# Kernel optimization log

Hardware: AMD Instinct MI355X
Metric: run time of the kernel (lower is better)

Reference implementation:

```python
import jax, jax.numpy as jnp
import numpy as np

N = 32768      # nodes
E = 524288     # edges (avg degree 16)
G = 512        # graphs in batch
F_IN = 64      # one-hot node-label dim
H = 128        # hidden_dim
C = 2          # num_classes (NCI1)
BN_EPS = 1e-3  # keras BatchNormalization default epsilon


def setup_inputs() -> dict:
    key = jax.random.key(0)
    ks = jax.random.split(key, 32)
    d = {}
    d["x"] = jax.random.normal(ks[0], (N, F_IN), jnp.float32)
    d["edge_weight"] = jax.random.uniform(ks[1], (E,), jnp.float32)
    i = 2
    din = F_IN
    for l in range(5):
        d[f"W1_{l}"] = jax.random.normal(ks[i], (din, H), jnp.float32) / np.float32(np.sqrt(din)); i += 1
        d[f"b1_{l}"] = jnp.zeros((H,), jnp.float32)
        d[f"W2_{l}"] = jax.random.normal(ks[i], (H, H), jnp.float32) / np.float32(np.sqrt(H)); i += 1
        d[f"b2_{l}"] = jnp.zeros((H,), jnp.float32)
        din = H
    for j in (1, 2, 3):  # bn1, bn2, bn3 (bn0/bn4 unused in original call())
        d[f"g{j}"] = jnp.ones((H,), jnp.float32)
        d[f"be{j}"] = jnp.zeros((H,), jnp.float32)
        d[f"m{j}"] = jnp.zeros((H,), jnp.float32)
        d[f"v{j}"] = jnp.ones((H,), jnp.float32)
    d["Wm1"] = jax.random.normal(ks[i], (5 * H, 128), jnp.float32) / np.float32(np.sqrt(5 * H)); i += 1
    d["bm1"] = jnp.zeros((128,), jnp.float32)
    d["Wm2"] = jax.random.normal(ks[i], (128, C), jnp.float32) / np.float32(np.sqrt(128.0)); i += 1
    d["bm2"] = jnp.zeros((C,), jnp.float32)
    d["edge_index"] = jax.random.randint(ks[i], (2, E), 0, N, dtype=jnp.int32); i += 1
    d["node_graph_index"] = jnp.sort(jax.random.randint(ks[i], (N,), 0, G, dtype=jnp.int32))
    return d


def reference(x, edge_weight,
              W1_0, b1_0, W2_0, b2_0,
              W1_1, b1_1, W2_1, b2_1,
              W1_2, b1_2, W2_2, b2_2,
              W1_3, b1_3, W2_3, b2_3,
              W1_4, b1_4, W2_4, b2_4,
              g1, be1, m1, v1,
              g2, be2, m2, v2,
              g3, be3, m3, v3,
              Wm1, bm1, Wm2, bm2,
              edge_index, node_graph_index):
    src, dst = edge_index[0], edge_index[1]

    def gin(h, W1, b1, W2, b2):
        # GIN with eps=0: h' = MLP(h + sum_{j in N(i)} w_ij * h_j)
        msg = h[dst] * edge_weight[:, None]              # [E, d]
        agg = jax.ops.segment_sum(msg, src, num_segments=N)
        h2 = h + agg
        return jax.nn.relu(h2 @ W1 + b1) @ W2 + b2

    def bn(h, g, be, m, v):  # inference-mode batchnorm
        return (h - m) * jax.lax.rsqrt(v + BN_EPS) * g + be

    h1 = gin(x, W1_0, b1_0, W2_0, b2_0)
    h2 = gin(bn(h1, g1, be1, m1, v1), W1_1, b1_1, W2_1, b2_1)
    h3 = gin(bn(h2, g1, be1, m1, v1), W1_2, b1_2, W2_2, b2_2)  # bn1 reused, as in source
    h4 = gin(bn(h3, g2, be2, m2, v2), W1_3, b1_3, W2_3, b2_3)
    h5 = gin(bn(h4, g3, be3, m3, v3), W1_4, b1_4, W2_4, b2_4)
    h5 = bn(h5, g3, be3, m3, v3)                                # bn3 reused, as in source

    pool = lambda h: jax.ops.segment_sum(h, node_graph_index, num_segments=G)
    hg = jnp.concatenate([pool(h1), pool(h2), pool(h3), pool(h4), pool(h5)], axis=-1)  # [G, 5H]
    # readout MLP (dropout inactive at inference)
    return jax.nn.relu(hg @ Wm1 + bm1) @ Wm2 + bm2  # [G, C]
```

## Files before the change

kernel.cpp:

```cpp
#include <hip/hip_runtime.h>
#include <hip/hip_bf16.h>

#define NN 32768
#define EE 524288
#define GG 512
#define CAP 48

typedef __bf16 bf16x8 __attribute__((ext_vector_type(8)));
typedef float  f32x4  __attribute__((ext_vector_type(4)));

static __device__ __forceinline__ float bf2f(unsigned short u) {
    union { unsigned int i; float f; } v; v.i = ((unsigned int)u) << 16; return v.f;
}
static __device__ __forceinline__ unsigned short f2bf(float f) {
    __bf16 b = (__bf16)f;
    return __builtin_bit_cast(unsigned short, b);
}
static __device__ __forceinline__ unsigned int pk2(float a, float b) {
    return (unsigned int)f2bf(a) | ((unsigned int)f2bf(b) << 16);
}
static __device__ __forceinline__ void fmaV(float* a, float w, uint4 hv) {
    a[0] += w * bf2f((unsigned short)(hv.x & 0xffff));
    a[1] += w * bf2f((unsigned short)(hv.x >> 16));
    a[2] += w * bf2f((unsigned short)(hv.y & 0xffff));
    a[3] += w * bf2f((unsigned short)(hv.y >> 16));
    a[4] += w * bf2f((unsigned short)(hv.z & 0xffff));
    a[5] += w * bf2f((unsigned short)(hv.z >> 16));
    a[6] += w * bf2f((unsigned short)(hv.w & 0xffff));
    a[7] += w * bf2f((unsigned short)(hv.w >> 16));
}
static __device__ __forceinline__ void fmaV(float* a, float w, uint2 hv) {
    a[0] += w * bf2f((unsigned short)(hv.x & 0xffff));
    a[1] += w * bf2f((unsigned short)(hv.x >> 16));
    a[2] += w * bf2f((unsigned short)(hv.y & 0xffff));
    a[3] += w * bf2f((unsigned short)(hv.y >> 16));
}

struct WJob { const float* in; unsigned short* out; int K; };
struct WJobs { WJob j[10]; };

__global__ __launch_bounds__(256) void build_kernel(WJobs jobs,
                                                    const int* __restrict__ src,
                                                    const int* __restrict__ dst,
                                                    const float* __restrict__ w,
                                                    int* __restrict__ cnt,
                                                    unsigned int* __restrict__ csr,
                                                    const float* __restrict__ x,
                                                    unsigned short* __restrict__ xb) {
    if (blockIdx.x < 2048) {
        int e = blockIdx.x * 256 + threadIdx.x;
        int s = src[e];
        int slot = atomicAdd(&cnt[s], 1);
        if (slot < CAP)
            csr[(size_t)s * CAP + slot] = (unsigned int)dst[e] | ((unsigned int)f2bf(w[e]) << 16);
    } else if (blockIdx.x < 2088) {
        int b = blockIdx.x - 2048;
        WJob jb = jobs.j[b >> 2];
        int quarter = b & 3;
        int per = jb.K * 128 / 4;
        for (int idx = quarter * per + threadIdx.x; idx < (quarter + 1) * per; idx += 256) {
            int k = idx >> 7, c = idx & 127;
            jb.out[c * jb.K + k] = f2bf(jb.in[idx]);
        }
    } else {
        int base = (blockIdx.x - 2088) * 4096 + threadIdx.x;
        #pragma unroll
        for (int k = 0; k < 16; ++k) {
            int idx = base + k * 256;
            xb[idx] = f2bf(x[idx]);
        }
    }
}

template<bool FIRST, bool LAST>
__global__ __launch_bounds__(256) void layer_kernel(
        const unsigned short* __restrict__ h_in,
        const int* __restrict__ cnt,
        const unsigned int* __restrict__ csr,
        const unsigned short* __restrict__ W1t,
        const float* __restrict__ b1,
        const unsigned short* __restrict__ W2t,
        const float* __restrict__ b2,
        const float* __restrict__ g, const float* __restrict__ be,
        const float* __restrict__ m, const float* __restrict__ v,
        const int* __restrict__ gidx,
        unsigned short* __restrict__ h_out,
        float* __restrict__ pools, int col_off) {

    constexpr int K1 = FIRST ? 64 : 128;
    constexpr int KS1 = K1 / 32;
    constexpr int CH = FIRST ? 4 : 8;

    __shared__ unsigned int smem[2176];
    __shared__ float sscale[128], sshift[128];
    __shared__ int scnt[16];
    __shared__ int sgid[16];

    unsigned int* A1 = smem;
    unsigned int* T  = smem + 16 * 68;
    float* OUT = (float*)smem;

    int tid = threadIdx.x;
    int wave = tid >> 6, lane = tid & 63;
    int mrow = lane & 15, quad = lane >> 4;

    if (tid < 128) {
        float sc = g[tid] * rsqrtf(v[tid] + 1e-3f);
        sscale[tid] = sc;
        sshift[tid] = be[tid] - m[tid] * sc;
    } else if (tid < 144) {
        sgid[tid - 128] = gidx[blockIdx.x * 16 + (tid - 128)];
    } else if (tid < 160) {
        int d = cnt[blockIdx.x * 16 + (tid - 144)];
        scnt[tid - 144] = (d > CAP) ? CAP : d;
    }
    __syncthreads();

    {
        int i4 = lane >> 4;
        int half = (lane >> 3) & 1;
        int sub8 = lane & 7;
        int gbase = lane & 56;
        int r = wave * 4 + i4;
        int node = blockIdx.x * 16 + r;
        int deg = scnt[r];
        int md = max(max(scnt[wave * 4], scnt[wave * 4 + 1]),
                     max(scnt[wave * 4 + 2], scnt[wave * 4 + 3]));
        int mc = (md + 7) >> 3;
        size_t ebase = (size_t)node * CAP;

        unsigned int ev[6];
        #pragma unroll
        for (int c = 0; c < 6; ++c) {
            int p = c * 8 + sub8;
            unsigned int e2 = 0;
            if (p < deg) e2 = csr[ebase + p];
            ev[c] = e2;
        }

        float acc[CH];
        #pragma unroll
        for (int c = 0; c < CH; ++c) acc[c] = 0.f;

        if (FIRST) {
            const uint2* hp = (const uint2*)h_in;
            uint2 pre[4]; float wv[4];
            #pragma unroll
            for (int k = 0; k < 4; ++k) {
                unsigned int e2 = (unsigned int)__shfl((int)ev[0], gbase | k);
                wv[k] = bf2f((unsigned short)(e2 >> 16));
                pre[k] = hp[(size_t)(e2 & 0xffffu) * 16 + half * 8 + sub8];
            }
            #pragma unroll
            for (int c = 0; c < 6; ++c) {
                if (c >= mc) break;
                #pragma unroll
                for (int j = 0; j < 8; ++j) {
                    int t = c * 8 + j;
                    fmaV(acc, wv[t & 3], pre[t & 3]);
                    int tn = t + 4, cn = tn >> 3, jn = tn & 7;
                    if (cn < 6) {
                        unsigned int e2 = (unsigned int)__shfl((int)ev[cn], gbase | jn);
                        wv[t & 3] = bf2f((unsigned short)(e2 >> 16));
                        pre[t & 3] = hp[(size_t)(e2 & 0xffffu) * 16 + half * 8 + sub8];
                    }
                }
            }
            uint2 selfv = hp[(size_t)node * 16 + half * 8 + sub8];
            acc[0] += bf2f((unsigned short)(selfv.x & 0xffff));
            acc[1] += bf2f((unsigned short)(selfv.x >> 16));
            acc[2] += bf2f((unsigned short)(selfv.y & 0xffff));
            acc[3] += bf2f((unsigned short)(selfv.y >> 16));
            *(uint2*)(A1 + r * 68 + half * 16 + sub8 * 2) =
                make_uint2(pk2(acc[0], acc[1]), pk2(acc[2], acc[3]));
        } else {
            const uint4* hp = (const uint4*)h_in;
            uint4 pre[4]; float wv[4];
            #pragma unroll
            for (int k = 0; k < 4; ++k) {
                unsigned int e2 = (unsigned int)__shfl((int)ev[0], gbase | k);
                wv[k] = bf2f((unsigned short)(e2 >> 16));
                pre[k] = hp[(size_t)(e2 & 0xffffu) * 16 + half * 8 + sub8];
            }
            #pragma unroll
            for (int c = 0; c < 6; ++c) {
                if (c >= mc) break;
                #pragma unroll
                for (int j = 0; j < 8; ++j) {
                    int t = c * 8 + j;
                    fmaV(acc, wv[t & 3], pre[t & 3]);
                    int tn = t + 4, cn = tn >> 3, jn = tn & 7;
                    if (cn < 6) {
                        unsigned int e2 = (unsigned int)__shfl((int)ev[cn], gbase | jn);
                        wv[t & 3] = bf2f((unsigned short)(e2 >> 16));
                        pre[t & 3] = hp[(size_t)(e2 & 0xffffu) * 16 + half * 8 + sub8];
                    }
                }
            }
            uint4 selfv = hp[(size_t)node * 16 + half * 8 + sub8];
            acc[0] += bf2f((unsigned short)(selfv.x & 0xffff));
            acc[1] += bf2f((unsigned short)(selfv.x >> 16));
            acc[2] += bf2f((unsigned short)(selfv.y & 0xffff));
            acc[3] += bf2f((unsigned short)(selfv.y >> 16));
            acc[4] += bf2f((unsigned short)(selfv.z & 0xffff));
            acc[5] += bf2f((unsigned short)(selfv.z >> 16));
            acc[6] += bf2f((unsigned short)(selfv.w & 0xffff));
            acc[7] += bf2f((unsigned short)(selfv.w >> 16));
            *(uint4*)(A1 + r * 68 + half * 32 + sub8 * 4) =
                make_uint4(pk2(acc[0], acc[1]), pk2(acc[2], acc[3]),
                           pk2(acc[4], acc[5]), pk2(acc[6], acc[7]));
        }
    }
    __syncthreads();

    const unsigned short* A1s = (const unsigned short*)A1;
    unsigned short* Ts = (unsigned short*)T;

    bf16x8 af[KS1];
    #pragma unroll
    for (int kk = 0; kk < KS1; ++kk)
        af[kk] = *(const bf16x8*)(A1s + mrow * 136 + kk * 32 + quad * 8);

    f32x4 acc1v[2];
    #pragma unroll
    for (int c = 0; c < 2; ++c) acc1v[c] = (f32x4){0.f, 0.f, 0.f, 0.f};
    #pragma unroll
    for (int c = 0; c < 2; ++c) {
        const bf16x8* Brow = (const bf16x8*)(W1t + (size_t)(wave * 32 + c * 16 + mrow) * K1);
        #pragma unroll
        for (int kk = 0; kk < KS1; ++kk)
            acc1v[c] = __builtin_amdgcn_mfma_f32_16x16x32_bf16(af[kk], Brow[kk * 4 + quad], acc1v[c], 0, 0, 0);
    }
    #pragma unroll
    for (int c = 0; c < 2; ++c) {
        int ocol = wave * 32 + c * 16 + mrow;
        float bv = b1[ocol];
        #pragma unroll
        for (int r = 0; r < 4; ++r)
            Ts[(quad * 4 + r) * 136 + ocol] = f2bf(fmaxf(acc1v[c][r] + bv, 0.f));
    }
    __syncthreads();

    bf16x8 a2f[4];
    #pragma unroll
    for (int kk = 0; kk < 4; ++kk)
        a2f[kk] = *(const bf16x8*)(Ts + mrow * 136 + kk * 32 + quad * 8);
    f32x4 acc2v[2];
    #pragma unroll
    for (int c = 0; c < 2; ++c) acc2v[c] = (f32x4){0.f, 0.f, 0.f, 0.f};
    #pragma unroll
    for (int c = 0; c < 2; ++c) {
        const bf16x8* Brow = (const bf16x8*)(W2t + (size_t)(wave * 32 + c * 16 + mrow) * 128);
        #pragma unroll
        for (int kk = 0; kk < 4; ++kk)
            acc2v[c] = __builtin_amdgcn_mfma_f32_16x16x32_bf16(a2f[kk], Brow[kk * 4 + quad], acc2v[c], 0, 0, 0);
    }
    __syncthreads();

    #pragma unroll
    for (int c = 0; c < 2; ++c) {
        int ocol = wave * 32 + c * 16 + mrow;
        float bv = b2[ocol];
        #pragma unroll
        for (int r = 0; r < 4; ++r)
            OUT[(quad * 4 + r) * 132 + ocol] = acc2v[c][r] + bv;
    }
    __syncthreads();

    if (!LAST) {
        int row = tid >> 4, q = tid & 15;
        const float* Op = OUT + row * 132 + q * 8;
        unsigned int pk[4];
        #pragma unroll
        for (int i = 0; i < 4; ++i) {
            int c0 = q * 8 + i * 2;
            float o0 = Op[i * 2]     * sscale[c0]     + sshift[c0];
            float o1 = Op[i * 2 + 1] * sscale[c0 + 1] + sshift[c0 + 1];
            pk[i] = pk2(o0, o1);
        }
        *(uint4*)(h_out + (size_t)(blockIdx.x * 16 + row) * 128 + q * 8) =
            make_uint4(pk[0], pk[1], pk[2], pk[3]);
    }

    {
        int col = tid & 127, half = tid >> 7;
        float sc = LAST ? sscale[col] : 1.f;
        float sh = LAST ? sshift[col] : 0.f;
        float accp = 0.f;
        int cur = sgid[half * 8];
        for (int r = half * 8; r < half * 8 + 8; ++r) {
            int gi = sgid[r];
            if (gi != cur) {
                atomicAdd(&pools[(size_t)cur * 640 + col_off + col], accp);
                accp = 0.f;
                cur = gi;
            }
            float val = OUT[r * 132 + col];
            accp += LAST ? (val * sc + sh) : val;
        }
        atomicAdd(&pools[(size_t)cur * 640 + col_off + col], accp);
    }
}

__global__ __launch_bounds__(128) void readout(const float* __restrict__ pools,
                                               const float* __restrict__ Wm1,
                                               const float* __restrict__ bm1,
                                               const float* __restrict__ Wm2,
                                               const float* __restrict__ bm2,
                                               float* __restrict__ out) {
    __shared__ float row[640];
    __shared__ float partial[4];
    int gb = blockIdx.x;
    for (int k = threadIdx.x; k < 640; k += 128) row[k] = pools[(size_t)gb * 640 + k];
    __syncthreads();
    int j = threadIdx.x;
    float acc = bm1[j];
    for (int k = 0; k < 640; ++k) acc += row[k] * Wm1[(size_t)k * 128 + j];
    acc = fmaxf(acc, 0.f);
    float p0 = acc * Wm2[j * 2], p1 = acc * Wm2[j * 2 + 1];
    #pragma unroll
    for (int off = 32; off; off >>= 1) { p0 += __shfl_down(p0, off); p1 += __shfl_down(p1, off); }
    int wave = j >> 6;
    if ((j & 63) == 0) { partial[wave * 2] = p0; partial[wave * 2 + 1] = p1; }
    __syncthreads();
    if (j == 0) {
        out[gb * 2]     = bm2[0] + partial[0] + partial[2];
        out[gb * 2 + 1] = bm2[1] + partial[1] + partial[3];
    }
}

extern "C" void kernel_launch(void* const* d_in, const int* in_sizes, int n_in,
                              void* d_out, int out_size, void* d_ws, size_t ws_size,
                              hipStream_t stream) {
    const float* x  = (const float*)d_in[0];
    const float* ew = (const float*)d_in[1];
    const float *W1[5], *b1[5], *W2[5], *b2[5];
    for (int l = 0; l < 5; ++l) {
        W1[l] = (const float*)d_in[2 + 4 * l];
        b1[l] = (const float*)d_in[3 + 4 * l];
        W2[l] = (const float*)d_in[4 + 4 * l];
        b2[l] = (const float*)d_in[5 + 4 * l];
    }
    const float *bg[3], *bb[3], *bm[3], *bv[3];
    for (int j = 0; j < 3; ++j) {
        bg[j] = (const float*)d_in[22 + 4 * j];
        bb[j] = (const float*)d_in[23 + 4 * j];
        bm[j] = (const float*)d_in[24 + 4 * j];
        bv[j] = (const float*)d_in[25 + 4 * j];
    }
    const float* Wm1 = (const float*)d_in[34];
    const float* bm1 = (const float*)d_in[35];
    const float* Wm2 = (const float*)d_in[36];
    const float* bm2 = (const float*)d_in[37];
    const int* edge_index = (const int*)d_in[38];
    const int* src = edge_index;
    const int* dst = edge_index + EE;
    const int* gidx = (const int*)d_in[39];

    char* p = (char*)d_ws;
    auto alloc = [&](size_t bytes) -> void* {
        void* r = (void*)p;
        p += (bytes + 255) & ~(size_t)255;
        return r;
    };
    unsigned int* csr  = (unsigned int*)alloc((size_t)NN * CAP * 4);
    int* cnt           = (int*)alloc(NN * 4);
    unsigned short* xb = (unsigned short*)alloc((size_t)NN * 64 * 2);
    unsigned short* hA = (unsigned short*)alloc((size_t)NN * 128 * 2);
    unsigned short* hB = (unsigned short*)alloc((size_t)NN * 128 * 2);
    float* pools = (float*)alloc((size_t)GG * 640 * 4);
    unsigned short* W1t[5], *W2t[5];
    for (int l = 0; l < 5; ++l) {
        W1t[l] = (unsigned short*)alloc((size_t)128 * 128 * 2);
        W2t[l] = (unsigned short*)alloc((size_t)128 * 128 * 2);
    }

    hipMemsetAsync(cnt, 0, NN * 4, stream);
    hipMemsetAsync(pools, 0, (size_t)GG * 640 * 4, stream);

    WJobs jobs;
    for (int l = 0; l < 5; ++l) {
        jobs.j[2 * l]     = WJob{W1[l], W1t[l], (l == 0) ? 64 : 128};
        jobs.j[2 * l + 1] = WJob{W2[l], W2t[l], 128};
    }
    build_kernel<<<2048 + 40 + 512, 256, 0, stream>>>(jobs, src, dst, ew, cnt, csr, x, xb);

    const int bnsel[5] = {0, 0, 1, 2, 2};

    layer_kernel<true, false><<<NN / 16, 256, 0, stream>>>(
        xb, cnt, csr, W1t[0], b1[0], W2t[0], b2[0],
        bg[0], bb[0], bm[0], bv[0], gidx, hA, pools, 0);

    const unsigned short* hin = hA;
    unsigned short* hout = hB;
    for (int l = 1; l < 5; ++l) {
        int s = bnsel[l];
        if (l < 4) {
            layer_kernel<false, false><<<NN / 16, 256, 0, stream>>>(
                hin, cnt, csr, W1t[l], b1[l], W2t[l], b2[l],
                bg[s], bb[s], bm[s], bv[s], gidx, hout, pools, l * 128);
        } else {
            layer_kernel<false, true><<<NN / 16, 256, 0, stream>>>(
                hin, cnt, csr, W1t[l], b1[l], W2t[l], b2[l],
                bg[s], bb[s], bm[s], bv[s], gidx, hout, pools, l * 128);
        }
        unsigned short* tmp = (unsigned short*)hin;
        hin = hout;
        hout = tmp;
    }

    readout<<<GG, 128, 0, stream>>>(pools, Wm1, bm1, Wm2, bm2, (float*)d_out);
}
```

Before: 336.3 us.

## Widen CSR rows to 64 with vectorized edge loads and 8-deep gather prefetch

Raises the per-node edge capacity to 64 and zero-fills the whole CSR slab, along with cnt and pools, in one memset. Each lane can then load its eight edge entries with two unguarded 128-bit loads instead of six guarded scalar loads. The gather loop now keeps eight neighbour rows in flight per chunk instead of four, and launch bounds request 4 blocks per CU. The trade-off is a larger memset and CSR footprint (64 entries per node) plus more registers for the deeper prefetch buffers, which could hurt occupancy.

```diff
diff --git a/kernel.cpp b/kernel.cpp
--- a/kernel.cpp
+++ b/kernel.cpp
@@ -4,7 +4,7 @@
 #define NN 32768
 #define EE 524288
 #define GG 512
-#define CAP 48
+#define CAP 64
 
 typedef __bf16 bf16x8 __attribute__((ext_vector_type(8)));
 typedef float  f32x4  __attribute__((ext_vector_type(4)));
@@ -73,7 +73,7 @@
 }
 
 template<bool FIRST, bool LAST>
-__global__ __launch_bounds__(256) void layer_kernel(
+__global__ __launch_bounds__(256, 4) void layer_kernel(
         const unsigned short* __restrict__ h_in,
         const int* __restrict__ cnt,
         const unsigned int* __restrict__ csr,
@@ -123,20 +123,14 @@
         int gbase = lane & 56;
         int r = wave * 4 + i4;
         int node = blockIdx.x * 16 + r;
-        int deg = scnt[r];
         int md = max(max(scnt[wave * 4], scnt[wave * 4 + 1]),
                      max(scnt[wave * 4 + 2], scnt[wave * 4 + 3]));
         int mc = (md + 7) >> 3;
         size_t ebase = (size_t)node * CAP;
 
-        unsigned int ev[6];
-        #pragma unroll
-        for (int c = 0; c < 6; ++c) {
-            int p = c * 8 + sub8;
-            unsigned int e2 = 0;
-            if (p < deg) e2 = csr[ebase + p];
-            ev[c] = e2;
-        }
+        uint4 evA = *(const uint4*)(csr + ebase + sub8 * 8);
+        uint4 evB = *(const uint4*)(csr + ebase + sub8 * 8 + 4);
+        unsigned int ev[8] = {evA.x, evA.y, evA.z, evA.w, evB.x, evB.y, evB.z, evB.w};
 
         float acc[CH];
         #pragma unroll
@@ -144,25 +138,24 @@
 
         if (FIRST) {
             const uint2* hp = (const uint2*)h_in;
-            uint2 pre[4]; float wv[4];
+            uint2 pre[8]; float wv[8];
             #pragma unroll
-            for (int k = 0; k < 4; ++k) {
-                unsigned int e2 = (unsigned int)__shfl((int)ev[0], gbase | k);
-                wv[k] = bf2f((unsigned short)(e2 >> 16));
-                pre[k] = hp[(size_t)(e2 & 0xffffu) * 16 + half * 8 + sub8];
+            for (int j = 0; j < 8; ++j) {
+                unsigned int e2 = (unsigned int)__shfl((int)ev[j], gbase);
+                wv[j] = bf2f((unsigned short)(e2 >> 16));
+                pre[j] = hp[(size_t)(e2 & 0xffffu) * 16 + half * 8 + sub8];
             }
             #pragma unroll
-            for (int c = 0; c < 6; ++c) {
+            for (int c = 0; c < 8; ++c) {
                 if (c >= mc) break;
+                bool pf = (c + 1 < mc);
                 #pragma unroll
                 for (int j = 0; j < 8; ++j) {
-                    int t = c * 8 + j;
-                    fmaV(acc, wv[t & 3], pre[t & 3]);
-                    int tn = t + 4, cn = tn >> 3, jn = tn & 7;
-                    if (cn < 6) {
-                        unsigned int e2 = (unsigned int)__shfl((int)ev[cn], gbase | jn);
-                        wv[t & 3] = bf2f((unsigned short)(e2 >> 16));
-                        pre[t & 3] = hp[(size_t)(e2 & 0xffffu) * 16 + half * 8 + sub8];
+                    fmaV(acc, wv[j], pre[j]);
+                    if (pf) {
+                        unsigned int e2 = (unsigned int)__shfl((int)ev[j], gbase | (c + 1));
+                        wv[j] = bf2f((unsigned short)(e2 >> 16));
+                        pre[j] = hp[(size_t)(e2 & 0xffffu) * 16 + half * 8 + sub8];
                     }
                 }
             }
@@ -175,25 +168,24 @@
                 make_uint2(pk2(acc[0], acc[1]), pk2(acc[2], acc[3]));
         } else {
             const uint4* hp = (const uint4*)h_in;
-            uint4 pre[4]; float wv[4];
+            uint4 pre[8]; float wv[8];
             #pragma unroll
-            for (int k = 0; k < 4; ++k) {
-                unsigned int e2 = (unsigned int)__shfl((int)ev[0], gbase | k);
-                wv[k] = bf2f((unsigned short)(e2 >> 16));
-                pre[k] = hp[(size_t)(e2 & 0xffffu) * 16 + half * 8 + sub8];
+            for (int j = 0; j < 8; ++j) {
+                unsigned int e2 = (unsigned int)__shfl((int)ev[j], gbase);
+                wv[j] = bf2f((unsigned short)(e2 >> 16));
+                pre[j] = hp[(size_t)(e2 & 0xffffu) * 16 + half * 8 + sub8];
             }
             #pragma unroll
-            for (int c = 0; c < 6; ++c) {
+            for (int c = 0; c < 8; ++c) {
                 if (c >= mc) break;
+                bool pf = (c + 1 < mc);
                 #pragma unroll
                 for (int j = 0; j < 8; ++j) {
-                    int t = c * 8 + j;
-                    fmaV(acc, wv[t & 3], pre[t & 3]);
-                    int tn = t + 4, cn = tn >> 3, jn = tn & 7;
-                    if (cn < 6) {
-                        unsigned int e2 = (unsigned int)__shfl((int)ev[cn], gbase | jn);
-                        wv[t & 3] = bf2f((unsigned short)(e2 >> 16));
-                        pre[t & 3] = hp[(size_t)(e2 & 0xffffu) * 16 + half * 8 + sub8];
+                    fmaV(acc, wv[j], pre[j]);
+                    if (pf) {
+                        unsigned int e2 = (unsigned int)__shfl((int)ev[j], gbase | (c + 1));
+                        wv[j] = bf2f((unsigned short)(e2 >> 16));
+                        pre[j] = hp[(size_t)(e2 & 0xffffu) * 16 + half * 8 + sub8];
                     }
                 }
             }
@@ -365,18 +357,18 @@
     };
     unsigned int* csr  = (unsigned int*)alloc((size_t)NN * CAP * 4);
     int* cnt           = (int*)alloc(NN * 4);
+    float* pools       = (float*)alloc((size_t)GG * 640 * 4);
+    size_t zspan = (size_t)(p - (char*)csr);
     unsigned short* xb = (unsigned short*)alloc((size_t)NN * 64 * 2);
     unsigned short* hA = (unsigned short*)alloc((size_t)NN * 128 * 2);
     unsigned short* hB = (unsigned short*)alloc((size_t)NN * 128 * 2);
-    float* pools = (float*)alloc((size_t)GG * 640 * 4);
     unsigned short* W1t[5], *W2t[5];
     for (int l = 0; l < 5; ++l) {
         W1t[l] = (unsigned short*)alloc((size_t)128 * 128 * 2);
         W2t[l] = (unsigned short*)alloc((size_t)128 * 128 * 2);
     }
 
-    hipMemsetAsync(cnt, 0, NN * 4, stream);
-    hipMemsetAsync(pools, 0, (size_t)GG * 640 * 4, stream);
+    hipMemsetAsync(csr, 0, zspan, stream);
 
     WJobs jobs;
     for (int l = 0; l < 5; ++l) {
```

After: 346.8 us. 3.1% more time.

## Double layer kernel block size and split each node's edges across two lane groups

Applied to the files above, without the earlier changes.

Layer kernels now launch 512 threads (8 waves) per 16-node block. In the gather, each wave handles 2 nodes instead of 4, and each node's edge list is split by parity between two 32-lane halves, whose partial sums are then combined with a cross-half shuffle. The MFMA stages give each wave one 16-column tile instead of two, and the BN/store and pooling epilogues are re-split across the larger block. The aim is more memory-level parallelism and shorter per-lane gather chains, at the cost of extra shuffles, more threads per block and possibly lower occupancy.

```diff
diff --git a/kernel.cpp b/kernel.cpp
--- a/kernel.cpp
+++ b/kernel.cpp
@@ -73,7 +73,7 @@
 }
 
 template<bool FIRST, bool LAST>
-__global__ __launch_bounds__(256) void layer_kernel(
+__global__ __launch_bounds__(512) void layer_kernel(
         const unsigned short* __restrict__ h_in,
         const int* __restrict__ cnt,
         const unsigned int* __restrict__ csr,
@@ -117,26 +117,24 @@
     __syncthreads();
 
     {
-        int i4 = lane >> 4;
+        int sub8 = lane & 7;
         int half = (lane >> 3) & 1;
-        int sub8 = lane & 7;
-        int gbase = lane & 56;
-        int r = wave * 4 + i4;
+        int nsel = (lane >> 4) & 1;
+        int epar = lane >> 5;
+        int r = wave * 2 + nsel;
         int node = blockIdx.x * 16 + r;
         int deg = scnt[r];
-        int md = max(max(scnt[wave * 4], scnt[wave * 4 + 1]),
-                     max(scnt[wave * 4 + 2], scnt[wave * 4 + 3]));
-        int mc = (md + 7) >> 3;
+        int md = max(scnt[wave * 2], scnt[wave * 2 + 1]);
+        int TT = (md + 1) >> 1;
         size_t ebase = (size_t)node * CAP;
 
         unsigned int ev[6];
         #pragma unroll
         for (int c = 0; c < 6; ++c) {
             int p = c * 8 + sub8;
-            unsigned int e2 = 0;
-            if (p < deg) e2 = csr[ebase + p];
-            ev[c] = e2;
-        }
+            ev[c] = (p < deg) ? csr[ebase + p] : 0u;
+        }
+        int bsrc = (lane & 16) | epar;
 
         float acc[CH];
         #pragma unroll
@@ -147,68 +145,72 @@
             uint2 pre[4]; float wv[4];
             #pragma unroll
             for (int k = 0; k < 4; ++k) {
-                unsigned int e2 = (unsigned int)__shfl((int)ev[0], gbase | k);
-                wv[k] = bf2f((unsigned short)(e2 >> 16));
-                pre[k] = hp[(size_t)(e2 & 0xffffu) * 16 + half * 8 + sub8];
-            }
-            #pragma unroll
-            for (int c = 0; c < 6; ++c) {
-                if (c >= mc) break;
-                #pragma unroll
-                for (int j = 0; j < 8; ++j) {
-                    int t = c * 8 + j;
-                    fmaV(acc, wv[t & 3], pre[t & 3]);
-                    int tn = t + 4, cn = tn >> 3, jn = tn & 7;
-                    if (cn < 6) {
-                        unsigned int e2 = (unsigned int)__shfl((int)ev[cn], gbase | jn);
-                        wv[t & 3] = bf2f((unsigned short)(e2 >> 16));
-                        pre[t & 3] = hp[(size_t)(e2 & 0xffffu) * 16 + half * 8 + sub8];
-                    }
+                if (k < TT) {
+                    unsigned int e2 = (unsigned int)__shfl((int)ev[(2 * k) >> 3], bsrc | ((2 * k) & 7));
+                    wv[k] = bf2f((unsigned short)(e2 >> 16));
+                    pre[k] = hp[(size_t)(e2 & 0xffffu) * 16 + half * 8 + sub8];
                 }
             }
-            uint2 selfv = hp[(size_t)node * 16 + half * 8 + sub8];
-            acc[0] += bf2f((unsigned short)(selfv.x & 0xffff));
-            acc[1] += bf2f((unsigned short)(selfv.x >> 16));
-            acc[2] += bf2f((unsigned short)(selfv.y & 0xffff));
-            acc[3] += bf2f((unsigned short)(selfv.y >> 16));
-            *(uint2*)(A1 + r * 68 + half * 16 + sub8 * 2) =
-                make_uint2(pk2(acc[0], acc[1]), pk2(acc[2], acc[3]));
+            #pragma unroll
+            for (int t = 0; t < 24; ++t) {
+                if (t >= TT) break;
+                fmaV(acc, wv[t & 3], pre[t & 3]);
+                int tn = t + 4;
+                if (tn < TT) {
+                    unsigned int e2 = (unsigned int)__shfl((int)ev[(2 * tn) >> 3], bsrc | ((2 * tn) & 7));
+                    wv[t & 3] = bf2f((unsigned short)(e2 >> 16));
+                    pre[t & 3] = hp[(size_t)(e2 & 0xffffu) * 16 + half * 8 + sub8];
+                }
+            }
+            #pragma unroll
+            for (int c = 0; c < 4; ++c) acc[c] += __shfl_xor(acc[c], 32);
+            if (epar == 0) {
+                uint2 sv = hp[(size_t)node * 16 + half * 8 + sub8];
+                acc[0] += bf2f((unsigned short)(sv.x & 0xffff));
+                acc[1] += bf2f((unsigned short)(sv.x >> 16));
+                acc[2] += bf2f((unsigned short)(sv.y & 0xffff));
+                acc[3] += bf2f((unsigned short)(sv.y >> 16));
+                *(uint2*)(A1 + r * 68 + (half * 8 + sub8) * 2) =
+                    make_uint2(pk2(acc[0], acc[1]), pk2(acc[2], acc[3]));
+            }
         } else {
             const uint4* hp = (const uint4*)h_in;
             uint4 pre[4]; float wv[4];
             #pragma unroll
             for (int k = 0; k < 4; ++k) {
-                unsigned int e2 = (unsigned int)__shfl((int)ev[0], gbase | k);
-                wv[k] = bf2f((unsigned short)(e2 >> 16));
-                pre[k] = hp[(size_t)(e2 & 0xffffu) * 16 + half * 8 + sub8];
-            }
-            #pragma unroll
-            for (int c = 0; c < 6; ++c) {
-                if (c >= mc) break;
-                #pragma unroll
-                for (int j = 0; j < 8; ++j) {
-                    int t = c * 8 + j;
-                    fmaV(acc, wv[t & 3], pre[t & 3]);
-                    int tn = t + 4, cn = tn >> 3, jn = tn & 7;
-                    if (cn < 6) {
-                        unsigned int e2 = (unsigned int)__shfl((int)ev[cn], gbase | jn);
-                        wv[t & 3] = bf2f((unsigned short)(e2 >> 16));
-                        pre[t & 3] = hp[(size_t)(e2 & 0xffffu) * 16 + half * 8 + sub8];
-                    }
+                if (k < TT) {
+                    unsigned int e2 = (unsigned int)__shfl((int)ev[(2 * k) >> 3], bsrc | ((2 * k) & 7));
+                    wv[k] = bf2f((unsigned short)(e2 >> 16));
+                    pre[k] = hp[(size_t)(e2 & 0xffffu) * 16 + half * 8 + sub8];
                 }
             }
-            uint4 selfv = hp[(size_t)node * 16 + half * 8 + sub8];
-            acc[0] += bf2f((unsigned short)(selfv.x & 0xffff));
-            acc[1] += bf2f((unsigned short)(selfv.x >> 16));
-            acc[2] += bf2f((unsigned short)(selfv.y & 0xffff));
-            acc[3] += bf2f((unsigned short)(selfv.y >> 16));
-            acc[4] += bf2f((unsigned short)(selfv.z & 0xffff));
-            acc[5] += bf2f((unsigned short)(selfv.z >> 16));
-            acc[6] += bf2f((unsigned short)(selfv.w & 0xffff));
-            acc[7] += bf2f((unsigned short)(selfv.w >> 16));
-            *(uint4*)(A1 + r * 68 + half * 32 + sub8 * 4) =
-                make_uint4(pk2(acc[0], acc[1]), pk2(acc[2], acc[3]),
-                           pk2(acc[4], acc[5]), pk2(acc[6], acc[7]));
+            #pragma unroll
+            for (int t = 0; t < 24; ++t) {
+                if (t >= TT) break;
+                fmaV(acc, wv[t & 3], pre[t & 3]);
+                int tn = t + 4;
+                if (tn < TT) {
+                    unsigned int e2 = (unsigned int)__shfl((int)ev[(2 * tn) >> 3], bsrc | ((2 * tn) & 7));
+                    wv[t & 3] = bf2f((unsigned short)(e2 >> 16));
+                    pre[t & 3] = hp[(size_t)(e2 & 0xffffu) * 16 + half * 8 + sub8];
+                }
+            }
+            #pragma unroll
+            for (int c = 0; c < 8; ++c) acc[c] += __shfl_xor(acc[c], 32);
+            if (epar == 0) {
+                uint4 sv = hp[(size_t)node * 16 + half * 8 + sub8];
+                acc[0] += bf2f((unsigned short)(sv.x & 0xffff));
+                acc[1] += bf2f((unsigned short)(sv.x >> 16));
+                acc[2] += bf2f((unsigned short)(sv.y & 0xffff));
+                acc[3] += bf2f((unsigned short)(sv.y >> 16));
+                acc[4] += bf2f((unsigned short)(sv.z & 0xffff));
+                acc[5] += bf2f((unsigned short)(sv.z >> 16));
+                acc[6] += bf2f((unsigned short)(sv.w & 0xffff));
+                acc[7] += bf2f((unsigned short)(sv.w >> 16));
+                *(uint4*)(A1 + r * 68 + half * 32 + sub8 * 4) =
+                    make_uint4(pk2(acc[0], acc[1]), pk2(acc[2], acc[3]),
+                               pk2(acc[4], acc[5]), pk2(acc[6], acc[7]));
+            }
         }
     }
     __syncthreads();
@@ -221,23 +223,19 @@
     for (int kk = 0; kk < KS1; ++kk)
         af[kk] = *(const bf16x8*)(A1s + mrow * 136 + kk * 32 + quad * 8);
 
-    f32x4 acc1v[2];
-    #pragma unroll
-    for (int c = 0; c < 2; ++c) acc1v[c] = (f32x4){0.f, 0.f, 0.f, 0.f};
-    #pragma unroll
-    for (int c = 0; c < 2; ++c) {
-        const bf16x8* Brow = (const bf16x8*)(W1t + (size_t)(wave * 32 + c * 16 + mrow) * K1);
+    f32x4 acc1v = (f32x4){0.f, 0.f, 0.f, 0.f};
+    {
+        const bf16x8* Brow = (const bf16x8*)(W1t + (size_t)(wave * 16 + mrow) * K1);
         #pragma unroll
         for (int kk = 0; kk < KS1; ++kk)
-            acc1v[c] = __builtin_amdgcn_mfma_f32_16x16x32_bf16(af[kk], Brow[kk * 4 + quad], acc1v[c], 0, 0, 0);
-    }
-    #pragma unroll
-    for (int c = 0; c < 2; ++c) {
-        int ocol = wave * 32 + c * 16 + mrow;
+            acc1v = __builtin_amdgcn_mfma_f32_16x16x32_bf16(af[kk], Brow[kk * 4 + quad], acc1v, 0, 0, 0);
+    }
+    {
+        int ocol = wave * 16 + mrow;
         float bv = b1[ocol];
         #pragma unroll
         for (int r = 0; r < 4; ++r)
-            Ts[(quad * 4 + r) * 136 + ocol] = f2bf(fmaxf(acc1v[c][r] + bv, 0.f));
+            Ts[(quad * 4 + r) * 136 + ocol] = f2bf(fmaxf(acc1v[r] + bv, 0.f));
     }
     __syncthreads();
 
@@ -245,50 +243,42 @@
     #pragma unroll
     for (int kk = 0; kk < 4; ++kk)
         a2f[kk] = *(const bf16x8*)(Ts + mrow * 136 + kk * 32 + quad * 8);
-    f32x4 acc2v[2];
-    #pragma unroll
-    for (int c = 0; c < 2; ++c) acc2v[c] = (f32x4){0.f, 0.f, 0.f, 0.f};
-    #pragma unroll
-    for (int c = 0; c < 2; ++c) {
-        const bf16x8* Brow = (const bf16x8*)(W2t + (size_t)(wave * 32 + c * 16 + mrow) * 128);
+    f32x4 acc2v = (f32x4){0.f, 0.f, 0.f, 0.f};
+    {
+        const bf16x8* Brow = (const bf16x8*)(W2t + (size_t)(wave * 16 + mrow) * 128);
         #pragma unroll
         for (int kk = 0; kk < 4; ++kk)
-            acc2v[c] = __builtin_amdgcn_mfma_f32_16x16x32_bf16(a2f[kk], Brow[kk * 4 + quad], acc2v[c], 0, 0, 0);
-    }
-    __syncthreads();
-
-    #pragma unroll
-    for (int c = 0; c < 2; ++c) {
-        int ocol = wave * 32 + c * 16 + mrow;
+            acc2v = __builtin_amdgcn_mfma_f32_16x16x32_bf16(a2f[kk], Brow[kk * 4 + quad], acc2v, 0, 0, 0);
+    }
+    __syncthreads();
+
+    {
+        int ocol = wave * 16 + mrow;
         float bv = b2[ocol];
         #pragma unroll
         for (int r = 0; r < 4; ++r)
-            OUT[(quad * 4 + r) * 132 + ocol] = acc2v[c][r] + bv;
+            OUT[(quad * 4 + r) * 132 + ocol] = acc2v[r] + bv;
     }
     __syncthreads();
 
     if (!LAST) {
-        int row = tid >> 4, q = tid & 15;
-        const float* Op = OUT + row * 132 + q * 8;
-        unsigned int pk[4];
-        #pragma unroll
-        for (int i = 0; i < 4; ++i) {
-            int c0 = q * 8 + i * 2;
-            float o0 = Op[i * 2]     * sscale[c0]     + sshift[c0];
-            float o1 = Op[i * 2 + 1] * sscale[c0 + 1] + sshift[c0 + 1];
-            pk[i] = pk2(o0, o1);
-        }
-        *(uint4*)(h_out + (size_t)(blockIdx.x * 16 + row) * 128 + q * 8) =
-            make_uint4(pk[0], pk[1], pk[2], pk[3]);
-    }
-
-    {
-        int col = tid & 127, half = tid >> 7;
+        int row = tid >> 5, q = tid & 31;
+        const float* Op = OUT + row * 132 + q * 4;
+        float o0 = Op[0] * sscale[q * 4 + 0] + sshift[q * 4 + 0];
+        float o1 = Op[1] * sscale[q * 4 + 1] + sshift[q * 4 + 1];
+        float o2 = Op[2] * sscale[q * 4 + 2] + sshift[q * 4 + 2];
+        float o3 = Op[3] * sscale[q * 4 + 3] + sshift[q * 4 + 3];
+        *(uint2*)(h_out + (size_t)(blockIdx.x * 16 + row) * 128 + q * 4) =
+            make_uint2(pk2(o0, o1), pk2(o2, o3));
+    }
+
+    {
+        int col = tid & 127, quarter = tid >> 7;
         float sc = LAST ? sscale[col] : 1.f;
         float sh = LAST ? sshift[col] : 0.f;
         float accp = 0.f;
-        int cur = sgid[half * 8];
-        for (int r = half * 8; r < half * 8 + 8; ++r) {
+        int cur = sgid[quarter * 4];
+        for (int r = quarter * 4; r < quarter * 4 + 4; ++r) {
             int gi = sgid[r];
             if (gi != cur) {
                 atomicAdd(&pools[(size_t)cur * 640 + col_off + col], accp);
@@ -365,10 +355,10 @@
     };
     unsigned int* csr  = (unsigned int*)alloc((size_t)NN * CAP * 4);
     int* cnt           = (int*)alloc(NN * 4);
+    float* pools       = (float*)alloc((size_t)GG * 640 * 4);
     unsigned short* xb = (unsigned short*)alloc((size_t)NN * 64 * 2);
     unsigned short* hA = (unsigned short*)alloc((size_t)NN * 128 * 2);
     unsigned short* hB = (unsigned short*)alloc((size_t)NN * 128 * 2);
-    float* pools = (float*)alloc((size_t)GG * 640 * 4);
     unsigned short* W1t[5], *W2t[5];
     for (int l = 0; l < 5; ++l) {
         W1t[l] = (unsigned short*)alloc((size_t)128 * 128 * 2);
@@ -387,7 +377,7 @@
 
     const int bnsel[5] = {0, 0, 1, 2, 2};
 
-    layer_kernel<true, false><<<NN / 16, 256, 0, stream>>>(
+    layer_kernel<true, false><<<NN / 16, 512, 0, stream>>>(
         xb, cnt, csr, W1t[0], b1[0], W2t[0], b2[0],
         bg[0], bb[0], bm[0], bv[0], gidx, hA, pools, 0);
 
@@ -396,11 +386,11 @@
     for (int l = 1; l < 5; ++l) {
         int s = bnsel[l];
         if (l < 4) {
-            layer_kernel<false, false><<<NN / 16, 256, 0, stream>>>(
+            layer_kernel<false, false><<<NN / 16, 512, 0, stream>>>(
                 hin, cnt, csr, W1t[l], b1[l], W2t[l], b2[l],
                 bg[s], bb[s], bm[s], bv[s], gidx, hout, pools, l * 128);
         } else {
-            layer_kernel<false, true><<<NN / 16, 256, 0, stream>>>(
+            layer_kernel<false, true><<<NN / 16, 512, 0, stream>>>(
                 hin, cnt, csr, W1t[l], b1[l], W2t[l], b2[l],
                 bg[s], bb[s], bm[s], bv[s], gidx, hout, pools, l * 128);
         }
```

Measured after the change: 542.0 us. +61.2%, slower.
